# Kernel tuning notes

Hardware: AMD Instinct MI355X
Metric: run time of the kernel (lower is better)

Reference implementation:

```python
import jax, jax.numpy as jnp
import numpy as np
from jax import lax

EPS = 1e-5

def _bn_train(x, gamma, beta):
    # BatchNorm2d in training mode: batch stats over (N,H,W), biased variance
    mean = jnp.mean(x, axis=(0, 2, 3), keepdims=True)
    var = jnp.mean((x - mean) ** 2, axis=(0, 2, 3), keepdims=True)
    xhat = (x - mean) * lax.rsqrt(var + EPS)
    return gamma[None, :, None, None] * xhat + beta[None, :, None, None]

def _binact(x):
    # forward: sign(x); backward (STE): identity where |x|<=1, zero elsewhere
    y = jnp.where(jnp.abs(x) > 1.0, lax.stop_gradient(x), x)
    return y + lax.stop_gradient(jnp.sign(y) - y)

def _binconv(x, w, padding):
    # per-output-channel alpha = mean(|w|) over (in,kh,kw); w_bin = sign(w)*alpha with STE
    alpha = jnp.mean(jnp.abs(w), axis=(1, 2, 3), keepdims=True)
    w_bin = lax.stop_gradient(jnp.sign(w) * alpha - w) + w
    return lax.conv_general_dilated(
        x, w_bin, window_strides=(1, 1),
        padding=[(padding, padding), (padding, padding)],
        dimension_numbers=("NCHW", "OIHW", "NCHW"))

def setup_inputs() -> dict:
    key = jax.random.key(0)
    ks = jax.random.split(key, 10)
    B, Cin, Cout, H, W, T = 32, 128, 256, 64, 64, 512
    x = jax.random.normal(ks[0], (B, Cin, H, W), jnp.float32)
    t = jax.random.normal(ks[1], (B, T), jnp.float32)
    # conv weights, kaiming-ish scale
    w1 = jax.random.normal(ks[2], (Cout, Cin, 3, 3), jnp.float32) * (1.0 / np.sqrt(Cin * 9))
    w2 = jax.random.normal(ks[3], (Cout, Cout, 3, 3), jnp.float32) * (1.0 / np.sqrt(Cout * 9))
    wskip = jax.random.normal(ks[4], (Cout, Cin, 1, 1), jnp.float32) * (1.0 / np.sqrt(Cin))
    gamma1 = 1.0 + 0.1 * jax.random.normal(ks[5], (Cin,), jnp.float32)
    beta1 = 0.1 * jax.random.normal(ks[6], (Cin,), jnp.float32)
    gamma2 = 1.0 + 0.1 * jax.random.normal(ks[7], (Cout,), jnp.float32)
    beta2 = 0.1 * jax.random.normal(ks[8], (Cout,), jnp.float32)
    tw = jax.random.normal(ks[9], (Cout, T), jnp.float32) * (1.0 / np.sqrt(T))
    tb = jnp.zeros((Cout,), jnp.float32)
    return {"x": x, "t": t, "w1": w1, "w2": w2, "wskip": wskip,
            "gamma1": gamma1, "beta1": beta1, "gamma2": gamma2, "beta2": beta2,
            "tw": tw, "tb": tb}

def reference(x, t, w1, w2, wskip, gamma1, beta1, gamma2, beta2, tw, tb):
    h = _binconv(_binact(_bn_train(x, gamma1, beta1)), w1, padding=1)
    temb = t @ tw.T + tb                      # [B, Cout]
    h = h + temb[:, :, None, None]
    h = _binconv(_binact(_bn_train(h, gamma2, beta2)), w2, padding=1)
    return h + _binconv(x, wskip, padding=0)
```

## Files before the change

### kernel.cpp

```cpp
#include <hip/hip_runtime.h>
#include <stdint.h>

typedef unsigned short u16;
typedef uint8_t u8;
typedef __attribute__((ext_vector_type(8))) short short8;
typedef __attribute__((ext_vector_type(4))) float f32x4;
typedef __attribute__((ext_vector_type(4))) int i32x4;

#define EPSF 1e-5f
#define LGKM0 asm volatile("s_waitcnt lgkmcnt(0)" ::: "memory")
#define VM0   asm volatile("s_waitcnt vmcnt(0)" ::: "memory")
#define VM4   asm volatile("s_waitcnt vmcnt(4)" ::: "memory")
#define BAR   __builtin_amdgcn_s_barrier()
#define GLL(src, dst) __builtin_amdgcn_global_load_lds(                     \
    (const __attribute__((address_space(1))) void*)(src),                   \
    (__attribute__((address_space(3))) void*)(dst), 16, 0, 0)

__device__ __forceinline__ u16 f2bf(float f) {
  uint32_t u = __float_as_uint(f);
  u += 0x7FFFu + ((u >> 16) & 1u);
  return (u16)(u >> 16);
}
__device__ __forceinline__ u8 sgn8(float y) {
  return y > 0.f ? (u8)1 : (y < 0.f ? (u8)0xFF : (u8)0);
}

__global__ void bn1_stage1(const float* __restrict__ x, float* __restrict__ p1) {
  int c = blockIdx.x >> 2, s = blockIdx.x & 3;
  int tid = threadIdx.x;
  float sum = 0.f, sq = 0.f;
  for (int n = s * 8; n < s * 8 + 8; ++n) {
    const f32x4* bp = (const f32x4*)(x + (((size_t)(n * 128 + c)) << 12));
    #pragma unroll 4
    for (int i = tid; i < 1024; i += 256) {
      f32x4 v = bp[i];
      sum += v[0] + v[1] + v[2] + v[3];
      sq  += v[0]*v[0] + v[1]*v[1] + v[2]*v[2] + v[3]*v[3];
    }
  }
  __shared__ float rs[256], rq[256];
  rs[tid] = sum; rq[tid] = sq; __syncthreads();
  for (int st = 128; st > 0; st >>= 1) {
    if (tid < st) { rs[tid] += rs[tid + st]; rq[tid] += rq[tid + st]; }
    __syncthreads();
  }
  if (tid == 0) { p1[blockIdx.x] = rs[0]; p1[512 + blockIdx.x] = rq[0]; }
}

__global__ void bn1_stage2(const float* __restrict__ p1, const float* __restrict__ g,
                           const float* __restrict__ b, float* __restrict__ sc,
                           float* __restrict__ off) {
  int c = threadIdx.x;
  float s = 0.f, q = 0.f;
  for (int k = 0; k < 4; ++k) { s += p1[c * 4 + k]; q += p1[512 + c * 4 + k]; }
  float mean = s * (1.f / 131072.f);
  float var  = q * (1.f / 131072.f) - mean * mean;
  float is = rsqrtf(var + EPSF);
  float scv = g[c] * is;
  sc[c] = scv;
  off[c] = b[c] - mean * scv;
}

__global__ void bn2_stage2b(const float* __restrict__ pS, const float* __restrict__ pQ,
                            const float* __restrict__ g, const float* __restrict__ bb,
                            float* __restrict__ sc, float* __restrict__ off) {
  int o = blockIdx.x, t = threadIdx.x;
  __shared__ float rs[256], rq[256];
  const float* ps = pS + (size_t)o * 1024;
  const float* pq = pQ + (size_t)o * 1024;
  float s = ps[t] + ps[t + 256] + ps[t + 512] + ps[t + 768];
  float q = pq[t] + pq[t + 256] + pq[t + 512] + pq[t + 768];
  rs[t] = s; rq[t] = q; __syncthreads();
  for (int st = 128; st > 0; st >>= 1) {
    if (t < st) { rs[t] += rs[t + st]; rq[t] += rq[t + st]; }
    __syncthreads();
  }
  if (t == 0) {
    float mean = rs[0] * (1.f / 131072.f);
    float var  = rq[0] * (1.f / 131072.f) - mean * mean;
    float is = rsqrtf(var + EPSF);
    float scv = g[o] * is;
    sc[o] = scv;
    off[o] = bb[o] - mean * scv;
  }
}

__device__ __forceinline__ float blk_reduce(float v, float* red) {
  int t = threadIdx.x;
  red[t] = v; __syncthreads();
  for (int st = 128; st > 0; st >>= 1) {
    if (t < st) red[t] += red[t + st];
    __syncthreads();
  }
  float r = red[0]; __syncthreads();
  return r;
}

__global__ void prep_weights(const float* __restrict__ w1, const float* __restrict__ w2,
                             const float* __restrict__ wsk, u8* __restrict__ w1s,
                             u8* __restrict__ w2s, u16* __restrict__ wskB,
                             float* __restrict__ alpha1, float* __restrict__ alpha2) {
  int o = blockIdx.x, t = threadIdx.x;
  int rg = o >> 6, ol = o & 63;
  __shared__ float red[256];
  float s = 0.f;
  for (int j = t; j < 1152; j += 256) s += fabsf(w1[(size_t)o * 1152 + j]);
  float a1 = blk_reduce(s, red) * (1.f / 1152.f);
  if (t == 0) alpha1[o] = a1;
  for (int j = t; j < 1152; j += 256) {
    int st = j >> 6, k = j & 63;
    int tap = st >> 1, cc = st & 1;
    int ch = cc * 64 + k;
    int g = (ol << 2) + ((k >> 4) ^ (ol & 3));
    w1s[(size_t)st * 16384 + rg * 4096 + g * 16 + (k & 15)] =
        sgn8(w1[(size_t)o * 1152 + ch * 9 + tap]);
  }
  s = 0.f;
  for (int j = t; j < 2304; j += 256) s += fabsf(w2[(size_t)o * 2304 + j]);
  float a2 = blk_reduce(s, red) * (1.f / 2304.f);
  if (t == 0) alpha2[o] = a2;
  for (int j = t; j < 2304; j += 256) {
    int st = j >> 6, k = j & 63;
    int c2 = st / 18, r = st % 18, tap = r >> 1, cc = r & 1;
    int ch = c2 * 128 + cc * 64 + k;
    int g = (ol << 2) + ((k >> 4) ^ (ol & 3));
    w2s[(size_t)st * 16384 + rg * 4096 + g * 16 + (k & 15)] =
        sgn8(w2[(size_t)o * 2304 + ch * 9 + tap]);
  }
  s = 0.f;
  for (int j = t; j < 128; j += 256) s += fabsf(wsk[o * 128 + j]);
  float ask = blk_reduce(s, red) * (1.f / 128.f);
  float ratio = ask / a2;
  for (int j = t; j < 128; j += 256) {
    int e = j >> 6, k = j & 63;
    float w = wsk[o * 128 + j];
    float v = w > 0.f ? ratio : (w < 0.f ? -ratio : 0.f);
    wskB[(size_t)e * 16384 + o * 64 + k] = f2bf(v);
  }
}

__global__ void temb_k(const float* __restrict__ t, const float* __restrict__ tw,
                       const float* __restrict__ tb, float* __restrict__ temb) {
  int bb = blockIdx.x, o = threadIdx.x;
  __shared__ float tl[512];
  tl[o] = t[bb * 512 + o];
  tl[o + 256] = t[bb * 512 + 256 + o];
  __syncthreads();
  float acc = tb[o];
  #pragma unroll 8
  for (int k = 0; k < 512; ++k) acc += tl[k] * tw[(size_t)o * 512 + k];
  temb[bb * 256 + o] = acc;
}

__global__ void border_zero(u8* __restrict__ Abuf) {
  u8* plane = Abuf + (size_t)blockIdx.x * 557568;
  int tid = threadIdx.x;
  i32x4 z = {};
  for (int idx = tid; idx < 260; idx += 256) {
    int row, px;
    if (idx < 66) { row = 0; px = idx; }
    else if (idx < 132) { row = 65; px = idx - 66; }
    else { int e = idx - 132; row = 1 + (e >> 1); px = (e & 1) * 65; }
    u8* p = plane + (size_t)(row * 66 + px) * 128;
    #pragma unroll
    for (int i = 0; i < 8; ++i) *(i32x4*)(p + i * 16) = z;
  }
}

__global__ void binact1(const float* __restrict__ x, const float* __restrict__ sc,
                        const float* __restrict__ off, u8* __restrict__ a1p,
                        u16* __restrict__ xb) {
  int b = blockIdx.x >> 6, y = blockIdx.x & 63, tid = threadIdx.x;
  __shared__ u8  ls[64 * 144];
  __shared__ u16 lx[64 * 136];
  int c = tid >> 1, x0 = (tid & 1) * 32;
  const float* src = x + (((size_t)(b * 128 + c)) << 12) + y * 64 + x0;
  float s0 = sc[c], o0 = off[c];
  #pragma unroll
  for (int i = 0; i < 32; i += 4) {
    f32x4 v = *(const f32x4*)(src + i);
    #pragma unroll
    for (int j = 0; j < 4; ++j) {
      int xc = x0 + i + j;
      float yv = s0 * v[j] + o0;
      ls[xc * 144 + c] = sgn8(yv);
      lx[xc * 136 + c] = f2bf(v[j]);
    }
  }
  __syncthreads();
  int xx = tid >> 2, cg = (tid & 3) * 32;
  u8*  pdst = a1p + ((size_t)b * 4356 + (y + 1) * 66 + xx + 1) * 128 + cg;
  u16* xdst = xb + ((size_t)blockIdx.x * 64 + xx) * 128 + cg;
  *(i32x4*)(pdst)      = *(const i32x4*)&ls[xx * 144 + cg];
  *(i32x4*)(pdst + 16) = *(const i32x4*)&ls[xx * 144 + cg + 16];
  #pragma unroll
  for (int i = 0; i < 32; i += 8)
    *(i32x4*)(xdst + i) = *(const i32x4*)&lx[xx * 136 + cg + i];
}

__global__ void binact2(const float* __restrict__ h, const float* __restrict__ sc,
                        const float* __restrict__ off, u8* __restrict__ a2p) {
  int b = blockIdx.x >> 6, y = blockIdx.x & 63, tid = threadIdx.x;
  __shared__ float s_sc[256], s_off[256];
  s_sc[tid] = sc[tid]; s_off[tid] = off[tid];
  __syncthreads();
  const f32x4* src = (const f32x4*)(h + (size_t)blockIdx.x * 16384);
  #pragma unroll 4
  for (int i = tid; i < 4096; i += 256) {
    f32x4 v = src[i];
    int px = i >> 6, c0 = (i & 63) * 4;
    int c2 = c0 >> 7, chm = c0 & 127;
    uint32_t p = (uint32_t)sgn8(s_sc[c0 + 0] * v[0] + s_off[c0 + 0]) |
                 ((uint32_t)sgn8(s_sc[c0 + 1] * v[1] + s_off[c0 + 1]) << 8) |
                 ((uint32_t)sgn8(s_sc[c0 + 2] * v[2] + s_off[c0 + 2]) << 16) |
                 ((uint32_t)sgn8(s_sc[c0 + 3] * v[3] + s_off[c0 + 3]) << 24);
    u8* dst = a2p + ((size_t)(b * 2 + c2) * 4356 + (y + 1) * 66 + px + 1) * 128 + chm;
    *(uint32_t*)dst = p;
  }
}

template <int NCHUNK, bool SKIP, bool ADD_TEMB, bool STATS, bool DIRECT>
__global__ __launch_bounds__(512, 4) void convk(
    const u8* __restrict__ Apl, const u16* __restrict__ xb,
    const u8* __restrict__ wS, const u16* __restrict__ wskB,
    const float* __restrict__ alpha, const float* __restrict__ temb,
    float* __restrict__ outp, float* __restrict__ pS, float* __restrict__ pQ) {
  constexpr int NS = NCHUNK * 18;
  __shared__ u8 smem[66560];
  u8* lA = smem;
  u8* lB = smem + 33792;
  const int tid = threadIdx.x;
  const int lane = tid & 63, w = tid >> 6, wm = w >> 2, wn = w & 3;
  const int kq = lane >> 4, li = lane & 15;

  const int bid = blockIdx.x;
  const int tile = (bid & 7) * 128 + (bid >> 3);
  const int m0 = tile * 128;
  const int b = m0 >> 12, row0 = (m0 >> 6) & 63;

  auto issueB = [&](int s) {
    const u8* src = wS + (size_t)s * 16384 + wn * 4096 + lane * 16;
    u8* dst = lB + (s & 1) * 16384 + wn * 4096;
    #pragma unroll
    for (int i = 0; i < 4; ++i) GLL(src + i * 1024, dst + i * 1024);
  };

  auto winLoad = [&](int c) {
    const u8* gp = Apl + (size_t)(b * NCHUNK + c) * 557568 + (size_t)row0 * 8448;
    #pragma unroll
    for (int k = 0; k < 4; ++k) {
      int g = tid + k * 512;
      int row = g / 528, rem = g - row * 528;
      int px = rem >> 3, sl = rem & 7;
      const u8* src = gp + (size_t)(row * 66 + px) * 128 + ((sl ^ (px & 7)) << 4);
      u8* dst = lA + (size_t)((tid & ~63) + k * 512) * 16;
      GLL(src, dst);
    }
    if (tid < 64) {
      int g = 2048 + tid;
      int rem = g - 3 * 528;
      int px = rem >> 3, sl = rem & 7;
      const u8* src = gp + (size_t)(3 * 66 + px) * 128 + ((sl ^ (px & 7)) << 4);
      u8* dst = lA + (size_t)2048 * 16;
      GLL(src, dst);
    }
  };

  const u8* pA[3][2];
  #pragma unroll
  for (int dx = 0; dx < 3; ++dx)
    #pragma unroll
    for (int cc = 0; cc < 2; ++cc)
      pA[dx][cc] = lA + (size_t)wm * 8448 + (li + dx) * 128 +
                   ((((cc << 2) + kq) ^ ((li + dx) & 7)) << 4);
  const u8* pB = lB + wn * 4096 + li * 64 + ((kq ^ (li & 3)) << 4);

  i32x4 acc[4][4] = {};

  auto compute = [&](int dy, int dx, int cc, int buf) {
    i32x4 av[4], bv[4];
    #pragma unroll
    for (int f = 0; f < 4; ++f)
      av[f] = *(const i32x4*)(pA[dx][cc] + dy * 8448 + f * 2048);
    #pragma unroll
    for (int f = 0; f < 4; ++f)
      bv[f] = *(const i32x4*)(pB + buf * 16384 + f * 1024);
    __builtin_amdgcn_s_setprio(1);
    #pragma unroll
    for (int mf = 0; mf < 4; ++mf)
      #pragma unroll
      for (int nf = 0; nf < 4; ++nf)
        acc[mf][nf] = __builtin_amdgcn_mfma_i32_16x16x64_i8(
            av[mf], bv[nf], acc[mf][nf], 0, 0, 0);
    __builtin_amdgcn_s_setprio(0);
  };

  winLoad(0);
  issueB(0);

  #pragma unroll
  for (int s = 0; s < NS; ++s) {
    const int t = s % 18, cc = t & 1, tap = t >> 1;
    if (s + 1 < NS) issueB(s + 1);
    if (s + 1 < NS) { VM4; } else { VM0; }
    if (t == 0) BAR;
    compute(tap / 3, tap % 3, cc, s & 1);
    LGKM0; BAR;
    if (t == 17 && s + 1 < NS) winLoad((s + 1) / 18);
  }

  f32x4 facc[4][4];
  if constexpr (SKIP) {
    #pragma unroll
    for (int mf = 0; mf < 4; ++mf)
      #pragma unroll
      for (int nf = 0; nf < 4; ++nf)
        #pragma unroll
        for (int r = 0; r < 4; ++r)
          facc[mf][nf][r] = (float)acc[mf][nf][r];
    const u8* pAs[2];
    const u8* pBs[2];
    #pragma unroll
    for (int ks = 0; ks < 2; ++ks) {
      pAs[ks] = lA + (wm * 64 + li) * 128 + ((((ks << 2) + kq) ^ (li & 7)) << 4);
      pBs[ks] = lB + (wn * 64 + li) * 128 + ((((ks << 2) + kq) ^ (li & 7)) << 4);
    }
    #pragma unroll
    for (int e = 0; e < 2; ++e) {
      #pragma unroll
      for (int k = 0; k < 2; ++k) {
        int g = tid + k * 512;
        int m = g >> 3, sl = g & 7;
        const u8* src = (const u8*)xb + (size_t)(m0 + m) * 256 + e * 128 +
                        ((sl ^ (m & 7)) << 4);
        u8* dst = lA + (size_t)((tid & ~63) + k * 512) * 16;
        GLL(src, dst);
      }
      i32x4 rS[4];
      const i32x4* gs = (const i32x4*)((const u8*)wskB + (size_t)e * 32768) + tid;
      #pragma unroll
      for (int k = 0; k < 4; ++k) rS[k] = gs[k * 512];
      VM0;
      #pragma unroll
      for (int k = 0; k < 4; ++k) {
        int g = tid + k * 512;
        int o = g >> 3, sl = g & 7;
        *(i32x4*)(lB + o * 128 + ((sl ^ (o & 7)) << 4)) = rS[k];
      }
      LGKM0; BAR;
      #pragma unroll
      for (int ks = 0; ks < 2; ++ks) {
        short8 av[4], bv[4];
        #pragma unroll
        for (int f = 0; f < 4; ++f) av[f] = *(const short8*)(pAs[ks] + f * 2048);
        #pragma unroll
        for (int f = 0; f < 4; ++f) bv[f] = *(const short8*)(pBs[ks] + f * 2048);
        __builtin_amdgcn_s_setprio(1);
        #pragma unroll
        for (int mf = 0; mf < 4; ++mf)
          #pragma unroll
          for (int nf = 0; nf < 4; ++nf)
            facc[mf][nf] = __builtin_amdgcn_mfma_f32_16x16x32_bf16(
                av[mf], bv[nf], facc[mf][nf], 0, 0, 0);
        __builtin_amdgcn_s_setprio(0);
      }
      if (e == 0) { LGKM0; BAR; }
    }
    LGKM0; BAR;
  }

  const int cb = wn * 64 + li;

  if constexpr (STATS) {
    float als[4], tas[4];
    #pragma unroll
    for (int nf = 0; nf < 4; ++nf) {
      int o = cb + nf * 16;
      als[nf] = alpha[o];
      tas[nf] = ADD_TEMB ? temb[b * 256 + o] : 0.f;
    }
    float ps[4] = {0.f, 0.f, 0.f, 0.f}, pq[4] = {0.f, 0.f, 0.f, 0.f};
    #pragma unroll
    for (int nf = 0; nf < 4; ++nf)
      #pragma unroll
      for (int mf = 0; mf < 4; ++mf)
        #pragma unroll
        for (int r = 0; r < 4; ++r) {
          float v = (float)acc[mf][nf][r] * als[nf] + tas[nf];
          ps[nf] += v; pq[nf] += v * v;
        }
    #pragma unroll
    for (int nf = 0; nf < 4; ++nf) {
      ps[nf] += __shfl_xor(ps[nf], 16); ps[nf] += __shfl_xor(ps[nf], 32);
      pq[nf] += __shfl_xor(pq[nf], 16); pq[nf] += __shfl_xor(pq[nf], 32);
    }
    float* reds = (float*)smem;
    float* redq = reds + 512;
    __syncthreads();
    if (lane < 16) {
      #pragma unroll
      for (int nf = 0; nf < 4; ++nf) {
        reds[wm * 256 + wn * 64 + nf * 16 + lane] = ps[nf];
        redq[wm * 256 + wn * 64 + nf * 16 + lane] = pq[nf];
      }
    }
    __syncthreads();
    if (tid < 256) {
      pS[(size_t)tid * 1024 + bid] = reds[tid] + reds[256 + tid];
      pQ[(size_t)tid * 1024 + bid] = redq[tid] + redq[256 + tid];
    }
    __syncthreads();
    float* ld = (float*)smem;
    #pragma unroll 1
    for (int p = 0; p < 2; ++p) {
      if (wm == p) {
        #pragma unroll
        for (int nf = 0; nf < 4; ++nf) {
          int colg0 = (cb + nf * 16) >> 2, c3 = li & 3;
          #pragma unroll
          for (int mf = 0; mf < 4; ++mf)
            #pragma unroll
            for (int r = 0; r < 4; ++r) {
              int rloc = mf * 16 + 4 * kq + r;
              float v = (float)acc[mf][nf][r] * als[nf] + tas[nf];
              ld[rloc * 256 + ((colg0 ^ kq) << 2) + c3] = v;
            }
        }
      }
      __syncthreads();
      #pragma unroll
      for (int it = 0; it < 8; ++it) {
        int flat = tid + it * 512;
        int row = flat >> 6, c4 = flat & 63;
        int c4p = c4 ^ ((row >> 2) & 3);
        f32x4 v = *(const f32x4*)&ld[row * 256 + c4p * 4];
        *(f32x4*)(outp + (size_t)(m0 + p * 64 + row) * 256 + c4 * 4) = v;
      }
      __syncthreads();
    }
  } else if constexpr (DIRECT) {
    float* tb2 = (float*)lA;
    float* obase = outp + (((size_t)(b * 256)) << 12) + (m0 & 4095);
    __syncthreads();
    #pragma unroll 1
    for (int c4 = 0; c4 < 4; ++c4) {
      if (wn == c4) {
        #pragma unroll
        for (int nf = 0; nf < 4; ++nf) {
          float al = alpha[c4 * 64 + nf * 16 + li];
          #pragma unroll
          for (int mf = 0; mf < 4; ++mf) {
            int cs = (li + nf * 16) ^ ((wm * 2 + (mf >> 1)) & 3);
            #pragma unroll
            for (int r = 0; r < 4; ++r)
              tb2[(wm * 64 + mf * 16 + 4 * kq + r) * 65 + cs] =
                  facc[mf][nf][r] * al;
          }
        }
      }
      __syncthreads();
      #pragma unroll
      for (int it = 0; it < 4; ++it) {
        int flat = tid + it * 512;
        int ch = flat >> 5, mg = flat & 31;
        int chs = ch ^ ((mg >> 3) & 3);
        f32x4 v;
        #pragma unroll
        for (int e = 0; e < 4; ++e) v[e] = tb2[(mg * 4 + e) * 65 + chs];
        *(f32x4*)(obase + (((size_t)(c4 * 64 + ch)) << 12) + mg * 4) = v;
      }
      __syncthreads();
    }
  }
}

extern "C" void kernel_launch(void* const* d_in, const int* in_sizes, int n_in,
                              void* d_out, int out_size, void* d_ws, size_t ws_size,
                              hipStream_t stream) {
  const float* x      = (const float*)d_in[0];
  const float* t      = (const float*)d_in[1];
  const float* w1     = (const float*)d_in[2];
  const float* w2     = (const float*)d_in[3];
  const float* wskip  = (const float*)d_in[4];
  const float* gamma1 = (const float*)d_in[5];
  const float* beta1  = (const float*)d_in[6];
  const float* gamma2 = (const float*)d_in[7];
  const float* beta2  = (const float*)d_in[8];
  const float* tw     = (const float*)d_in[9];
  const float* tb     = (const float*)d_in[10];
  float* out = (float*)d_out;

  uint8_t* base = (uint8_t*)d_ws;
  size_t off = 0;
  auto alloc = [&](size_t bytes) {
    void* p = base + off;
    off += (bytes + 255) & ~(size_t)255;
    return p;
  };
  u8* Abuf     = (u8*)alloc((size_t)96 * 557568);
  u8* a1p      = Abuf;
  u8* a2p      = Abuf + (size_t)32 * 557568;
  u16* xb      = (u16*)alloc((size_t)131072 * 128 * 2);
  float* h     = (float*)alloc((size_t)131072 * 256 * 4);
  u8* w1s      = (u8*)alloc((size_t)18 * 16384);
  u8* w2s      = (u8*)alloc((size_t)36 * 16384);
  u16* wskB    = (u16*)alloc((size_t)2 * 16384 * 2);
  float* temb  = (float*)alloc(32 * 256 * 4);
  float* alpha1 = (float*)alloc(256 * 4);
  float* alpha2 = (float*)alloc(256 * 4);
  float* p1    = (float*)alloc(1024 * 4);
  float* pS    = (float*)alloc((size_t)256 * 1024 * 4);
  float* pQ    = (float*)alloc((size_t)256 * 1024 * 4);
  float* sc1   = (float*)alloc(128 * 4);
  float* off1  = (float*)alloc(128 * 4);
  float* sc2   = (float*)alloc(256 * 4);
  float* off2  = (float*)alloc(256 * 4);

  border_zero<<<96, 256, 0, stream>>>(Abuf);

  bn1_stage1<<<512, 256, 0, stream>>>(x, p1);
  bn1_stage2<<<1, 128, 0, stream>>>(p1, gamma1, beta1, sc1, off1);
  prep_weights<<<256, 256, 0, stream>>>(w1, w2, wskip, w1s, w2s, wskB, alpha1, alpha2);
  temb_k<<<32, 256, 0, stream>>>(t, tw, tb, temb);
  binact1<<<2048, 256, 0, stream>>>(x, sc1, off1, a1p, xb);

  convk<1, false, true, true, false><<<1024, 512, 0, stream>>>(
      a1p, xb, w1s, (const u16*)nullptr, alpha1, temb, h, pS, pQ);

  bn2_stage2b<<<256, 256, 0, stream>>>(pS, pQ, gamma2, beta2, sc2, off2);
  binact2<<<2048, 256, 0, stream>>>(h, sc2, off2, a2p);

  convk<2, true, false, false, true><<<1024, 512, 0, stream>>>(
      a2p, xb, w2s, wskB, alpha2, (const float*)nullptr, out,
      (float*)nullptr, (float*)nullptr);

  (void)in_sizes; (void)n_in; (void)out_size; (void)ws_size;
}
```

Before: 306.6 us.

## Load conv weight fragments directly into registers, drop LDS staging and barriers

The weight prep kernel now stores the binarized and skip weights in a per-lane fragment order, so each MFMA lane can fetch its B operands straight from global memory into registers. The conv kernel no longer stages weights through LDS with double-buffered global_load_lds, and the per-step barriers and LDS waits are removed; barriers remain only around window reloads. This cuts LDS traffic and synchronisation in the main loop. In exchange it adds VGPR pressure and relies on the L2 cache to serve repeated weight reads across many blocks.

```diff
diff --git a/kernel.cpp b/kernel.cpp
--- a/kernel.cpp
+++ b/kernel.cpp
@@ -97,11 +97,11 @@
 }
 
 __global__ void prep_weights(const float* __restrict__ w1, const float* __restrict__ w2,
-                             const float* __restrict__ wsk, u8* __restrict__ w1s,
-                             u8* __restrict__ w2s, u16* __restrict__ wskB,
+                             const float* __restrict__ wsk, u8* __restrict__ w1r,
+                             u8* __restrict__ w2r, u16* __restrict__ wskr,
                              float* __restrict__ alpha1, float* __restrict__ alpha2) {
   int o = blockIdx.x, t = threadIdx.x;
-  int rg = o >> 6, ol = o & 63;
+  int rg = o >> 6, nf = (o >> 4) & 3, li = o & 15;
   __shared__ float red[256];
   float s = 0.f;
   for (int j = t; j < 1152; j += 256) s += fabsf(w1[(size_t)o * 1152 + j]);
@@ -111,9 +111,9 @@
     int st = j >> 6, k = j & 63;
     int tap = st >> 1, cc = st & 1;
     int ch = cc * 64 + k;
-    int g = (ol << 2) + ((k >> 4) ^ (ol & 3));
-    w1s[(size_t)st * 16384 + rg * 4096 + g * 16 + (k & 15)] =
-        sgn8(w1[(size_t)o * 1152 + ch * 9 + tap]);
+    size_t idx = ((size_t)((st * 4 + rg) * 64 + (k >> 4) * 16 + li)) * 64 +
+                 nf * 16 + (k & 15);
+    w1r[idx] = sgn8(w1[(size_t)o * 1152 + ch * 9 + tap]);
   }
   s = 0.f;
   for (int j = t; j < 2304; j += 256) s += fabsf(w2[(size_t)o * 2304 + j]);
@@ -123,19 +123,21 @@
     int st = j >> 6, k = j & 63;
     int c2 = st / 18, r = st % 18, tap = r >> 1, cc = r & 1;
     int ch = c2 * 128 + cc * 64 + k;
-    int g = (ol << 2) + ((k >> 4) ^ (ol & 3));
-    w2s[(size_t)st * 16384 + rg * 4096 + g * 16 + (k & 15)] =
-        sgn8(w2[(size_t)o * 2304 + ch * 9 + tap]);
+    size_t idx = ((size_t)((st * 4 + rg) * 64 + (k >> 4) * 16 + li)) * 64 +
+                 nf * 16 + (k & 15);
+    w2r[idx] = sgn8(w2[(size_t)o * 2304 + ch * 9 + tap]);
   }
   s = 0.f;
   for (int j = t; j < 128; j += 256) s += fabsf(wsk[o * 128 + j]);
   float ask = blk_reduce(s, red) * (1.f / 128.f);
   float ratio = ask / a2;
   for (int j = t; j < 128; j += 256) {
-    int e = j >> 6, k = j & 63;
+    int e = j >> 6, c = j & 63;
+    int ks = c >> 5, kq = (c >> 3) & 3, jj = c & 7;
     float w = wsk[o * 128 + j];
     float v = w > 0.f ? ratio : (w < 0.f ? -ratio : 0.f);
-    wskB[(size_t)e * 16384 + o * 64 + k] = f2bf(v);
+    wskr[((size_t)((e * 4 + rg) * 64 + kq * 16 + li)) * 64 + (ks * 4 + nf) * 8 + jj] =
+        f2bf(v);
   }
 }
 
@@ -222,13 +224,12 @@
 template <int NCHUNK, bool SKIP, bool ADD_TEMB, bool STATS, bool DIRECT>
 __global__ __launch_bounds__(512, 4) void convk(
     const u8* __restrict__ Apl, const u16* __restrict__ xb,
-    const u8* __restrict__ wS, const u16* __restrict__ wskB,
+    const u8* __restrict__ wB, const u16* __restrict__ wskr,
     const float* __restrict__ alpha, const float* __restrict__ temb,
     float* __restrict__ outp, float* __restrict__ pS, float* __restrict__ pQ) {
   constexpr int NS = NCHUNK * 18;
   __shared__ u8 smem[66560];
   u8* lA = smem;
-  u8* lB = smem + 33792;
   const int tid = threadIdx.x;
   const int lane = tid & 63, w = tid >> 6, wm = w >> 2, wn = w & 3;
   const int kq = lane >> 4, li = lane & 15;
@@ -238,11 +239,12 @@
   const int m0 = tile * 128;
   const int b = m0 >> 12, row0 = (m0 >> 6) & 63;
 
-  auto issueB = [&](int s) {
-    const u8* src = wS + (size_t)s * 16384 + wn * 4096 + lane * 16;
-    u8* dst = lB + (s & 1) * 16384 + wn * 4096;
-    #pragma unroll
-    for (int i = 0; i < 4; ++i) GLL(src + i * 1024, dst + i * 1024);
+  i32x4 rB[2][4];
+  const i32x4* wlane = (const i32x4*)(wB + ((size_t)wn * 64 + lane) * 64);
+  auto loadB = [&](int s, int slot) {
+    const i32x4* src = wlane + (size_t)s * 1024;
+    #pragma unroll
+    for (int i = 0; i < 4; ++i) rB[slot][i] = src[i];
   };
 
   auto winLoad = [&](int c) {
@@ -273,40 +275,39 @@
     for (int cc = 0; cc < 2; ++cc)
       pA[dx][cc] = lA + (size_t)wm * 8448 + (li + dx) * 128 +
                    ((((cc << 2) + kq) ^ ((li + dx) & 7)) << 4);
-  const u8* pB = lB + wn * 4096 + li * 64 + ((kq ^ (li & 3)) << 4);
 
   i32x4 acc[4][4] = {};
 
-  auto compute = [&](int dy, int dx, int cc, int buf) {
-    i32x4 av[4], bv[4];
+  auto compute = [&](int dy, int dx, int cc, int slot) {
+    i32x4 av[4];
     #pragma unroll
     for (int f = 0; f < 4; ++f)
       av[f] = *(const i32x4*)(pA[dx][cc] + dy * 8448 + f * 2048);
-    #pragma unroll
-    for (int f = 0; f < 4; ++f)
-      bv[f] = *(const i32x4*)(pB + buf * 16384 + f * 1024);
     __builtin_amdgcn_s_setprio(1);
     #pragma unroll
     for (int mf = 0; mf < 4; ++mf)
       #pragma unroll
       for (int nf = 0; nf < 4; ++nf)
         acc[mf][nf] = __builtin_amdgcn_mfma_i32_16x16x64_i8(
-            av[mf], bv[nf], acc[mf][nf], 0, 0, 0);
+            av[mf], rB[slot][nf], acc[mf][nf], 0, 0, 0);
     __builtin_amdgcn_s_setprio(0);
   };
 
   winLoad(0);
-  issueB(0);
+  loadB(0, 0);
+  VM4;
+  BAR;
 
   #pragma unroll
   for (int s = 0; s < NS; ++s) {
     const int t = s % 18, cc = t & 1, tap = t >> 1;
-    if (s + 1 < NS) issueB(s + 1);
-    if (s + 1 < NS) { VM4; } else { VM0; }
-    if (t == 0) BAR;
+    if (s + 1 < NS) { loadB(s + 1, (s + 1) & 1); VM4; } else { VM0; }
     compute(tap / 3, tap % 3, cc, s & 1);
-    LGKM0; BAR;
-    if (t == 17 && s + 1 < NS) winLoad((s + 1) / 18);
+    if (NCHUNK > 1 && t == 17 && s + 1 < NS) {
+      LGKM0; BAR;
+      winLoad((s + 1) / 18);
+      VM0; BAR;
+    }
   }
 
   f32x4 facc[4][4];
@@ -319,12 +320,10 @@
         for (int r = 0; r < 4; ++r)
           facc[mf][nf][r] = (float)acc[mf][nf][r];
     const u8* pAs[2];
-    const u8* pBs[2];
-    #pragma unroll
-    for (int ks = 0; ks < 2; ++ks) {
+    #pragma unroll
+    for (int ks = 0; ks < 2; ++ks)
       pAs[ks] = lA + (wm * 64 + li) * 128 + ((((ks << 2) + kq) ^ (li & 7)) << 4);
-      pBs[ks] = lB + (wn * 64 + li) * 128 + ((((ks << 2) + kq) ^ (li & 7)) << 4);
-    }
+    LGKM0; BAR;
     #pragma unroll
     for (int e = 0; e < 2; ++e) {
       #pragma unroll
@@ -336,37 +335,27 @@
         u8* dst = lA + (size_t)((tid & ~63) + k * 512) * 16;
         GLL(src, dst);
       }
-      i32x4 rS[4];
-      const i32x4* gs = (const i32x4*)((const u8*)wskB + (size_t)e * 32768) + tid;
-      #pragma unroll
-      for (int k = 0; k < 4; ++k) rS[k] = gs[k * 512];
-      VM0;
-      #pragma unroll
-      for (int k = 0; k < 4; ++k) {
-        int g = tid + k * 512;
-        int o = g >> 3, sl = g & 7;
-        *(i32x4*)(lB + o * 128 + ((sl ^ (o & 7)) << 4)) = rS[k];
-      }
-      LGKM0; BAR;
+      const u16* bbase = wskr + ((size_t)(e * 4 + wn) * 64 + lane) * 64;
+      short8 sb[8];
+      #pragma unroll
+      for (int i = 0; i < 8; ++i) sb[i] = *(const short8*)(bbase + i * 8);
+      VM0; BAR;
       #pragma unroll
       for (int ks = 0; ks < 2; ++ks) {
-        short8 av[4], bv[4];
+        short8 av[4];
         #pragma unroll
         for (int f = 0; f < 4; ++f) av[f] = *(const short8*)(pAs[ks] + f * 2048);
-        #pragma unroll
-        for (int f = 0; f < 4; ++f) bv[f] = *(const short8*)(pBs[ks] + f * 2048);
         __builtin_amdgcn_s_setprio(1);
         #pragma unroll
         for (int mf = 0; mf < 4; ++mf)
           #pragma unroll
           for (int nf = 0; nf < 4; ++nf)
             facc[mf][nf] = __builtin_amdgcn_mfma_f32_16x16x32_bf16(
-                av[mf], bv[nf], facc[mf][nf], 0, 0, 0);
+                av[mf], sb[ks * 4 + nf], facc[mf][nf], 0, 0, 0);
         __builtin_amdgcn_s_setprio(0);
       }
       if (e == 0) { LGKM0; BAR; }
     }
-    LGKM0; BAR;
   }
 
   const int cb = wn * 64 + li;
@@ -502,9 +491,9 @@
   u8* a2p      = Abuf + (size_t)32 * 557568;
   u16* xb      = (u16*)alloc((size_t)131072 * 128 * 2);
   float* h     = (float*)alloc((size_t)131072 * 256 * 4);
-  u8* w1s      = (u8*)alloc((size_t)18 * 16384);
-  u8* w2s      = (u8*)alloc((size_t)36 * 16384);
-  u16* wskB    = (u16*)alloc((size_t)2 * 16384 * 2);
+  u8* w1r      = (u8*)alloc((size_t)18 * 16384);
+  u8* w2r      = (u8*)alloc((size_t)36 * 16384);
+  u16* wskr    = (u16*)alloc((size_t)2 * 16384 * 2);
   float* temb  = (float*)alloc(32 * 256 * 4);
   float* alpha1 = (float*)alloc(256 * 4);
   float* alpha2 = (float*)alloc(256 * 4);
@@ -520,18 +509,18 @@
 
   bn1_stage1<<<512, 256, 0, stream>>>(x, p1);
   bn1_stage2<<<1, 128, 0, stream>>>(p1, gamma1, beta1, sc1, off1);
-  prep_weights<<<256, 256, 0, stream>>>(w1, w2, wskip, w1s, w2s, wskB, alpha1, alpha2);
+  prep_weights<<<256, 256, 0, stream>>>(w1, w2, wskip, w1r, w2r, wskr, alpha1, alpha2);
   temb_k<<<32, 256, 0, stream>>>(t, tw, tb, temb);
   binact1<<<2048, 256, 0, stream>>>(x, sc1, off1, a1p, xb);
 
   convk<1, false, true, true, false><<<1024, 512, 0, stream>>>(
-      a1p, xb, w1s, (const u16*)nullptr, alpha1, temb, h, pS, pQ);
+      a1p, xb, w1r, (const u16*)nullptr, alpha1, temb, h, pS, pQ);
 
   bn2_stage2b<<<256, 256, 0, stream>>>(pS, pQ, gamma2, beta2, sc2, off2);
   binact2<<<2048, 256, 0, stream>>>(h, sc2, off2, a2p);
 
   convk<2, true, false, false, true><<<1024, 512, 0, stream>>>(
-      a2p, xb, w2s, wskB, alpha2, (const float*)nullptr, out,
+      a2p, xb, w2r, wskr, alpha2, (const float*)nullptr, out,
       (float*)nullptr, (float*)nullptr);
 
   (void)in_sizes; (void)n_in; (void)out_size; (void)ws_size;
```

After: 352.4 us. 1.15x slower.

## Shrink conv tiles to one image row per 256-thread block and restructure pipeline

Applied to the files above, without the earlier changes.

The binary convolution kernel moves from 512-thread blocks covering two image rows (128 pixels) to 256-thread blocks covering one row (64 pixels), doubling the grid to 2048 blocks. The weight pipeline prefetches two stages ahead and drops the per-stage barrier, and window reloads between channel chunks become explicit synchronised phases. BN2 partial statistics are now written per block without a cross-wave reduction, and the stage-2 reducer reads a transposed layout. Smaller tiles give less A/B reuse per block and more halo reloads, traded for more blocks, higher occupancy and fewer barriers.

```diff
diff --git a/kernel.cpp b/kernel.cpp
--- a/kernel.cpp
+++ b/kernel.cpp
@@ -66,10 +66,13 @@
                             float* __restrict__ sc, float* __restrict__ off) {
   int o = blockIdx.x, t = threadIdx.x;
   __shared__ float rs[256], rq[256];
-  const float* ps = pS + (size_t)o * 1024;
-  const float* pq = pQ + (size_t)o * 1024;
-  float s = ps[t] + ps[t + 256] + ps[t + 512] + ps[t + 768];
-  float q = pq[t] + pq[t + 256] + pq[t + 512] + pq[t + 768];
+  float s = 0.f, q = 0.f;
+  #pragma unroll
+  for (int k = 0; k < 8; ++k) {
+    size_t j = t + k * 256;
+    s += pS[j * 256 + o];
+    q += pQ[j * 256 + o];
+  }
   rs[t] = s; rq[t] = q; __syncthreads();
   for (int st = 128; st > 0; st >>= 1) {
     if (t < st) { rs[t] += rs[t + st]; rq[t] += rq[t + st]; }
@@ -220,7 +223,7 @@
 }
 
 template <int NCHUNK, bool SKIP, bool ADD_TEMB, bool STATS, bool DIRECT>
-__global__ __launch_bounds__(512, 4) void convk(
+__global__ __launch_bounds__(256, 2) void convk(
     const u8* __restrict__ Apl, const u16* __restrict__ xb,
     const u8* __restrict__ wS, const u16* __restrict__ wskB,
     const float* __restrict__ alpha, const float* __restrict__ temb,
@@ -228,15 +231,15 @@
   constexpr int NS = NCHUNK * 18;
   __shared__ u8 smem[66560];
   u8* lA = smem;
-  u8* lB = smem + 33792;
+  u8* lB = smem + 25344;
   const int tid = threadIdx.x;
-  const int lane = tid & 63, w = tid >> 6, wm = w >> 2, wn = w & 3;
+  const int lane = tid & 63, wn = tid >> 6;
   const int kq = lane >> 4, li = lane & 15;
 
   const int bid = blockIdx.x;
-  const int tile = (bid & 7) * 128 + (bid >> 3);
-  const int m0 = tile * 128;
-  const int b = m0 >> 12, row0 = (m0 >> 6) & 63;
+  const int tile = (bid & 7) * 256 + (bid >> 3);
+  const int m0 = tile * 64;
+  const int b = tile >> 6, y = tile & 63;
 
   auto issueB = [&](int s) {
     const u8* src = wS + (size_t)s * 16384 + wn * 4096 + lane * 16;
@@ -246,23 +249,22 @@
   };
 
   auto winLoad = [&](int c) {
-    const u8* gp = Apl + (size_t)(b * NCHUNK + c) * 557568 + (size_t)row0 * 8448;
-    #pragma unroll
-    for (int k = 0; k < 4; ++k) {
-      int g = tid + k * 512;
+    const u8* gp = Apl + (size_t)(b * NCHUNK + c) * 557568 + (size_t)y * 8448;
+    #pragma unroll
+    for (int k = 0; k < 6; ++k) {
+      int g = tid + k * 256;
       int row = g / 528, rem = g - row * 528;
       int px = rem >> 3, sl = rem & 7;
       const u8* src = gp + (size_t)(row * 66 + px) * 128 + ((sl ^ (px & 7)) << 4);
-      u8* dst = lA + (size_t)((tid & ~63) + k * 512) * 16;
+      u8* dst = lA + (size_t)((tid & ~63) + k * 256) * 16;
       GLL(src, dst);
     }
-    if (tid < 64) {
-      int g = 2048 + tid;
-      int rem = g - 3 * 528;
+    if (tid < 48) {
+      int g = 1536 + tid;
+      int rem = g - 1056;
       int px = rem >> 3, sl = rem & 7;
-      const u8* src = gp + (size_t)(3 * 66 + px) * 128 + ((sl ^ (px & 7)) << 4);
-      u8* dst = lA + (size_t)2048 * 16;
-      GLL(src, dst);
+      const u8* src = gp + (size_t)(2 * 66 + px) * 128 + ((sl ^ (px & 7)) << 4);
+      GLL(src, lA + (size_t)1536 * 16);
     }
   };
 
@@ -271,7 +273,7 @@
   for (int dx = 0; dx < 3; ++dx)
     #pragma unroll
     for (int cc = 0; cc < 2; ++cc)
-      pA[dx][cc] = lA + (size_t)wm * 8448 + (li + dx) * 128 +
+      pA[dx][cc] = lA + (li + dx) * 128 +
                    ((((cc << 2) + kq) ^ ((li + dx) & 7)) << 4);
   const u8* pB = lB + wn * 4096 + li * 64 + ((kq ^ (li & 3)) << 4);
 
@@ -297,16 +299,22 @@
 
   winLoad(0);
   issueB(0);
+  issueB(1);
+  VM4;
+  BAR;
 
   #pragma unroll
   for (int s = 0; s < NS; ++s) {
+    if (NCHUNK > 1 && s > 0 && (s % 18) == 0) {
+      LGKM0; BAR;
+      winLoad(s / 18);
+      VM0; BAR;
+    }
     const int t = s % 18, cc = t & 1, tap = t >> 1;
-    if (s + 1 < NS) issueB(s + 1);
-    if (s + 1 < NS) { VM4; } else { VM0; }
-    if (t == 0) BAR;
+    if (s + 2 < NS) { VM4; } else { VM0; }
     compute(tap / 3, tap % 3, cc, s & 1);
-    LGKM0; BAR;
-    if (t == 17 && s + 1 < NS) winLoad((s + 1) / 18);
+    LGKM0;
+    if (s + 2 < NS) issueB(s + 2);
   }
 
   f32x4 facc[4][4];
@@ -322,28 +330,29 @@
     const u8* pBs[2];
     #pragma unroll
     for (int ks = 0; ks < 2; ++ks) {
-      pAs[ks] = lA + (wm * 64 + li) * 128 + ((((ks << 2) + kq) ^ (li & 7)) << 4);
+      pAs[ks] = lA + li * 128 + ((((ks << 2) + kq) ^ (li & 7)) << 4);
       pBs[ks] = lB + (wn * 64 + li) * 128 + ((((ks << 2) + kq) ^ (li & 7)) << 4);
     }
+    LGKM0; BAR;
     #pragma unroll
     for (int e = 0; e < 2; ++e) {
       #pragma unroll
       for (int k = 0; k < 2; ++k) {
-        int g = tid + k * 512;
+        int g = tid + k * 256;
         int m = g >> 3, sl = g & 7;
         const u8* src = (const u8*)xb + (size_t)(m0 + m) * 256 + e * 128 +
                         ((sl ^ (m & 7)) << 4);
-        u8* dst = lA + (size_t)((tid & ~63) + k * 512) * 16;
+        u8* dst = lA + (size_t)((tid & ~63) + k * 256) * 16;
         GLL(src, dst);
       }
-      i32x4 rS[4];
+      i32x4 rS[8];
       const i32x4* gs = (const i32x4*)((const u8*)wskB + (size_t)e * 32768) + tid;
       #pragma unroll
-      for (int k = 0; k < 4; ++k) rS[k] = gs[k * 512];
+      for (int k = 0; k < 8; ++k) rS[k] = gs[k * 256];
       VM0;
       #pragma unroll
-      for (int k = 0; k < 4; ++k) {
-        int g = tid + k * 512;
+      for (int k = 0; k < 8; ++k) {
+        int g = tid + k * 256;
         int o = g >> 3, sl = g & 7;
         *(i32x4*)(lB + o * 128 + ((sl ^ (o & 7)) << 4)) = rS[k];
       }
@@ -361,12 +370,11 @@
           #pragma unroll
           for (int nf = 0; nf < 4; ++nf)
             facc[mf][nf] = __builtin_amdgcn_mfma_f32_16x16x32_bf16(
-                av[mf], bv[nf], facc[mf][nf], 0, 0, 0);
+                av[mf], bv[ks * 4 + nf - ks * 4 + nf == nf ? nf : nf], facc[mf][nf], 0, 0, 0);
         __builtin_amdgcn_s_setprio(0);
       }
       if (e == 0) { LGKM0; BAR; }
     }
-    LGKM0; BAR;
   }
 
   const int cb = wn * 64 + li;
@@ -394,49 +402,38 @@
       ps[nf] += __shfl_xor(ps[nf], 16); ps[nf] += __shfl_xor(ps[nf], 32);
       pq[nf] += __shfl_xor(pq[nf], 16); pq[nf] += __shfl_xor(pq[nf], 32);
     }
-    float* reds = (float*)smem;
-    float* redq = reds + 512;
-    __syncthreads();
     if (lane < 16) {
       #pragma unroll
       for (int nf = 0; nf < 4; ++nf) {
-        reds[wm * 256 + wn * 64 + nf * 16 + lane] = ps[nf];
-        redq[wm * 256 + wn * 64 + nf * 16 + lane] = pq[nf];
-      }
-    }
-    __syncthreads();
-    if (tid < 256) {
-      pS[(size_t)tid * 1024 + bid] = reds[tid] + reds[256 + tid];
-      pQ[(size_t)tid * 1024 + bid] = redq[tid] + redq[256 + tid];
+        pS[(size_t)bid * 256 + wn * 64 + nf * 16 + lane] = ps[nf];
+        pQ[(size_t)bid * 256 + wn * 64 + nf * 16 + lane] = pq[nf];
+      }
     }
     __syncthreads();
     float* ld = (float*)smem;
-    #pragma unroll 1
-    for (int p = 0; p < 2; ++p) {
-      if (wm == p) {
-        #pragma unroll
-        for (int nf = 0; nf < 4; ++nf) {
-          int colg0 = (cb + nf * 16) >> 2, c3 = li & 3;
+    {
+      int colg0_base = cb >> 2, c3 = li & 3;
+      #pragma unroll
+      for (int nf = 0; nf < 4; ++nf) {
+        int colg0 = colg0_base + nf * 4;
+        #pragma unroll
+        for (int mf = 0; mf < 4; ++mf)
           #pragma unroll
-          for (int mf = 0; mf < 4; ++mf)
-            #pragma unroll
-            for (int r = 0; r < 4; ++r) {
-              int rloc = mf * 16 + 4 * kq + r;
-              float v = (float)acc[mf][nf][r] * als[nf] + tas[nf];
-              ld[rloc * 256 + ((colg0 ^ kq) << 2) + c3] = v;
-            }
-        }
-      }
-      __syncthreads();
-      #pragma unroll
-      for (int it = 0; it < 8; ++it) {
-        int flat = tid + it * 512;
-        int row = flat >> 6, c4 = flat & 63;
-        int c4p = c4 ^ ((row >> 2) & 3);
-        f32x4 v = *(const f32x4*)&ld[row * 256 + c4p * 4];
-        *(f32x4*)(outp + (size_t)(m0 + p * 64 + row) * 256 + c4 * 4) = v;
-      }
-      __syncthreads();
+          for (int r = 0; r < 4; ++r) {
+            int rloc = mf * 16 + 4 * kq + r;
+            float v = (float)acc[mf][nf][r] * als[nf] + tas[nf];
+            ld[rloc * 256 + ((colg0 ^ kq) << 2) + c3] = v;
+          }
+      }
+    }
+    __syncthreads();
+    #pragma unroll
+    for (int it = 0; it < 16; ++it) {
+      int flat = tid + it * 256;
+      int row = flat >> 6, c4 = flat & 63;
+      int c4p = c4 ^ ((row >> 2) & 3);
+      f32x4 v = *(const f32x4*)&ld[row * 256 + c4p * 4];
+      *(f32x4*)(outp + (size_t)(m0 + row) * 256 + c4 * 4) = v;
     }
   } else if constexpr (DIRECT) {
     float* tb2 = (float*)lA;
@@ -450,19 +447,18 @@
           float al = alpha[c4 * 64 + nf * 16 + li];
           #pragma unroll
           for (int mf = 0; mf < 4; ++mf) {
-            int cs = (li + nf * 16) ^ ((wm * 2 + (mf >> 1)) & 3);
+            int cs = (li + nf * 16) ^ ((mf >> 1) & 3);
             #pragma unroll
             for (int r = 0; r < 4; ++r)
-              tb2[(wm * 64 + mf * 16 + 4 * kq + r) * 65 + cs] =
-                  facc[mf][nf][r] * al;
+              tb2[(mf * 16 + 4 * kq + r) * 65 + cs] = facc[mf][nf][r] * al;
           }
         }
       }
       __syncthreads();
       #pragma unroll
       for (int it = 0; it < 4; ++it) {
-        int flat = tid + it * 512;
-        int ch = flat >> 5, mg = flat & 31;
+        int flat = tid + it * 256;
+        int ch = flat >> 4, mg = flat & 15;
         int chs = ch ^ ((mg >> 3) & 3);
         f32x4 v;
         #pragma unroll
@@ -509,8 +505,8 @@
   float* alpha1 = (float*)alloc(256 * 4);
   float* alpha2 = (float*)alloc(256 * 4);
   float* p1    = (float*)alloc(1024 * 4);
-  float* pS    = (float*)alloc((size_t)256 * 1024 * 4);
-  float* pQ    = (float*)alloc((size_t)256 * 1024 * 4);
+  float* pS    = (float*)alloc((size_t)2048 * 256 * 4);
+  float* pQ    = (float*)alloc((size_t)2048 * 256 * 4);
   float* sc1   = (float*)alloc(128 * 4);
   float* off1  = (float*)alloc(128 * 4);
   float* sc2   = (float*)alloc(256 * 4);
@@ -524,13 +520,13 @@
   temb_k<<<32, 256, 0, stream>>>(t, tw, tb, temb);
   binact1<<<2048, 256, 0, stream>>>(x, sc1, off1, a1p, xb);
 
-  convk<1, false, true, true, false><<<1024, 512, 0, stream>>>(
+  convk<1, false, true, true, false><<<2048, 256, 0, stream>>>(
       a1p, xb, w1s, (const u16*)nullptr, alpha1, temb, h, pS, pQ);
 
   bn2_stage2b<<<256, 256, 0, stream>>>(pS, pQ, gamma2, beta2, sc2, off2);
   binact2<<<2048, 256, 0, stream>>>(h, sc2, off2, a2p);
 
-  convk<2, true, false, false, true><<<1024, 512, 0, stream>>>(
+  convk<2, true, false, false, true><<<2048, 256, 0, stream>>>(
       a2p, xb, w2s, wskB, alpha2, (const float*)nullptr, out,
       (float*)nullptr, (float*)nullptr);
 
```

Result: faster. 289.0 us (-5.8%).
